# Performance work log

Hardware: AMD Instinct MI355X
Metric: run time of the kernel (lower is better)

## Reference

```python
import jax, jax.numpy as jnp
import numpy as np

RMS_EPS = 1e-8
Q_EPS = 1e-5

def rms_norm(x):
    # RMSNorm without learnable scale, as in BitNet reference BitLinear
    return x * jax.lax.rsqrt(jnp.mean(x * x, axis=-1, keepdims=True) + RMS_EPS)

def activation_quant(x):
    # per-token absmax int8 quant/dequant
    scale = 127.0 / jnp.clip(jnp.max(jnp.abs(x), axis=-1, keepdims=True), Q_EPS)
    return jnp.clip(jnp.round(x * scale), -128, 127) / scale

def weight_quant(w):
    # ternary absmean quant/dequant
    scale = 1.0 / jnp.clip(jnp.mean(jnp.abs(w)), Q_EPS)
    return jnp.clip(jnp.round(w * scale), -1, 1) / scale

def bitlinear(x, w):
    # forward path of BitLinear: RMSNorm -> quantized matmul (STE is identity in fwd)
    xn = rms_norm(x)
    xq = xn + jax.lax.stop_gradient(activation_quant(xn) - xn)
    wq = w + jax.lax.stop_gradient(weight_quant(w) - w)
    return jnp.einsum('bsh,oh->bso', xq, wq)

def setup_inputs() -> dict:
    key = jax.random.key(0)
    k1, k2, k3 = jax.random.split(key, 3)
    H, I = 2048, 8192  # hidden_size, intermediate_size = 4*H
    x = jax.random.normal(k1, (4, 2048, H), jnp.float32)
    w_gate = jax.random.normal(k2, (2 * I, H), jnp.float32) * 0.02
    w_down = jax.random.normal(k3, (H, I), jnp.float32) * 0.02
    return {"x": x, "w_gate": w_gate, "w_down": w_down}

def reference(x, w_gate, w_down):
    y = bitlinear(x, w_gate)          # [B,S,2I]
    gate, v = jnp.split(y, 2, axis=-1)
    return bitlinear(jax.nn.silu(gate) * v, w_down)  # [B,S,H]
```

## Files before the change

kernel.cpp:

```cpp
#include <hip/hip_runtime.h>


using char8  = __attribute__((ext_vector_type(8))) signed char;
using int4v  = __attribute__((ext_vector_type(4))) int;
using half8  = __attribute__((ext_vector_type(8))) _Float16;

__device__ __forceinline__ void glds16(const void* g, void* l) {
  __builtin_amdgcn_global_load_lds((const __attribute__((address_space(1))) void*)g,
                                   (__attribute__((address_space(3))) void*)l, 16, 0, 0);
}

#define SB0() __builtin_amdgcn_sched_barrier(0)

__global__ __launch_bounds__(256) void reduce_abs_kernel(
    const float4* __restrict__ w, float* __restrict__ partials, int n4) {
  int t = threadIdx.x;
  int gid = blockIdx.x * 256 + t;
  int stride = gridDim.x * 256;
  float s = 0.f;
  for (int i = gid; i < n4; i += stride) {
    float4 u = w[i];
    s += fabsf(u.x) + fabsf(u.y) + fabsf(u.z) + fabsf(u.w);
  }
  __shared__ float sm[256];
  sm[t] = s; __syncthreads();
  for (int off = 128; off > 0; off >>= 1) {
    if (t < off) sm[t] += sm[t + off];
    __syncthreads();
  }
  if (t == 0) partials[blockIdx.x] = sm[0];
}

__global__ __launch_bounds__(256) void finalize_kernel(
    const float* __restrict__ pf, float* __restrict__ scales) {
  __shared__ float sm[256];
  int t = threadIdx.x;
  float s = pf[t] + pf[t + 256] + pf[t + 512] + pf[t + 768];
  sm[t] = s; __syncthreads();
  for (int off = 128; off > 0; off >>= 1) {
    if (t < off) sm[t] += sm[t + off];
    __syncthreads();
  }
  if (t == 0) {
    float c = fmaxf(sm[0] / 33554432.0f, 1e-5f);
    scales[0] = c; scales[2] = 1.0f / c;
  }
  __syncthreads();
  s = pf[1024 + t] + pf[1280 + t] + pf[1536 + t] + pf[1792 + t];
  sm[t] = s; __syncthreads();
  for (int off = 128; off > 0; off >>= 1) {
    if (t < off) sm[t] += sm[t + off];
    __syncthreads();
  }
  if (t == 0) {
    float c = fmaxf(sm[0] / 16777216.0f, 1e-5f);
    scales[1] = c; scales[3] = 1.0f / c;
  }
}

__global__ __launch_bounds__(256) void quant_weight_kernel(
    const float4* __restrict__ w, char8* __restrict__ wq,
    const float* __restrict__ invp, int n8) {
  float inv = *invp;
  int stride = gridDim.x * 256;
  for (int i = blockIdx.x * 256 + threadIdx.x; i < n8; i += stride) {
    float4 a = w[2 * i], b = w[2 * i + 1];
    float v[8] = {a.x, a.y, a.z, a.w, b.x, b.y, b.z, b.w};
    char8 o;
#pragma unroll
    for (int j = 0; j < 8; ++j) {
      float q = rintf(v[j] * inv);
      q = fminf(fmaxf(q, -1.f), 1.f);
      o[j] = (signed char)(int)q;
    }
    wq[i] = o;
  }
}

__global__ __launch_bounds__(256) void act_quant_f32_kernel(
    const float* __restrict__ in, signed char* __restrict__ out,
    float* __restrict__ fscale) {
  const int token = blockIdx.x, t = threadIdx.x;
  const float4* row = (const float4*)(in + (size_t)token * 2048);
  float4 a = row[2 * t], b = row[2 * t + 1];
  float v[8] = {a.x, a.y, a.z, a.w, b.x, b.y, b.z, b.w};
  float ss = 0.f, am = 0.f;
#pragma unroll
  for (int j = 0; j < 8; ++j) { ss += v[j] * v[j]; am = fmaxf(am, fabsf(v[j])); }
  __shared__ float s1[256], s2[256];
  s1[t] = ss; s2[t] = am; __syncthreads();
  for (int off = 128; off > 0; off >>= 1) {
    if (t < off) { s1[t] += s1[t + off]; s2[t] = fmaxf(s2[t], s2[t + off]); }
    __syncthreads();
  }
  float r = 1.0f / sqrtf(s1[0] * (1.0f / 2048.0f) + 1e-8f);
  float f = fmaxf(s2[0] * r, 1e-5f);
  float s = 127.0f / f;
  if (t == 0) fscale[token] = f * (1.0f / 127.0f);
  char8 o;
#pragma unroll
  for (int j = 0; j < 8; ++j) {
    float q = rintf((v[j] * r) * s);
    q = fminf(fmaxf(q, -128.f), 127.f);
    o[j] = (signed char)(int)q;
  }
  ((char8*)(out + (size_t)token * 2048))[t] = o;
}

__global__ __launch_bounds__(256) void act_quant_h_kernel(
    const _Float16* __restrict__ in, signed char* __restrict__ out,
    float* __restrict__ fscale) {
  const int token = blockIdx.x, t = threadIdx.x;
  const half8* row = (const half8*)(in + (size_t)token * 8192);
  float v[32];
  float ss = 0.f, am = 0.f;
#pragma unroll
  for (int c = 0; c < 4; ++c) {
    half8 u = row[c * 256 + t];
#pragma unroll
    for (int j = 0; j < 8; ++j) {
      float f = (float)u[j]; v[c * 8 + j] = f;
      ss += f * f; am = fmaxf(am, fabsf(f));
    }
  }
  __shared__ float s1[256], s2[256];
  s1[t] = ss; s2[t] = am; __syncthreads();
  for (int off = 128; off > 0; off >>= 1) {
    if (t < off) { s1[t] += s1[t + off]; s2[t] = fmaxf(s2[t], s2[t + off]); }
    __syncthreads();
  }
  float r = 1.0f / sqrtf(s1[0] * (1.0f / 8192.0f) + 1e-8f);
  float f = fmaxf(s2[0] * r, 1e-5f);
  float s = 127.0f / f;
  if (t == 0) fscale[token] = f * (1.0f / 127.0f);
#pragma unroll
  for (int c = 0; c < 4; ++c) {
    char8 o;
#pragma unroll
    for (int j = 0; j < 8; ++j) {
      float q = rintf((v[c * 8 + j] * r) * s);
      q = fminf(fmaxf(q, -128.f), 127.f);
      o[j] = (signed char)(int)q;
    }
    ((char8*)(out + (size_t)token * 8192))[c * 256 + t] = o;
  }
}

__global__ __launch_bounds__(512, 2) void gemm1_kernel(
    const signed char* __restrict__ A,
    const signed char* __restrict__ B,
    const float* __restrict__ f1, const float* __restrict__ cgp,
    _Float16* __restrict__ Z) {
  constexpr int K = 2048, I = 8192, NT = K / 64;
  constexpr int ASZ = 16384, BUF = 32768;
  __shared__ __align__(16) signed char Ls[3 * BUF];
  const int t0 = blockIdx.y * 256, n0 = blockIdx.x * 128;
  const int tid = threadIdx.x, w = tid >> 6, l = tid & 63;
  const int wr = w >> 2, wc = w & 3;
  const int lrow = l & 15, lchunk = (l >> 4) * 16;

  int4v ag[8][2], av[8][2];
#pragma unroll
  for (int i = 0; i < 8; ++i)
#pragma unroll
    for (int j = 0; j < 2; ++j) { ag[i][j] = {0,0,0,0}; av[i][j] = {0,0,0,0}; }

  const signed char* src[4];
  int dst[4];
  src[0] = A + (size_t)(t0 + w * 16 + lrow) * K + lchunk;       dst[0] = w * 1024;
  src[1] = A + (size_t)(t0 + (w + 8) * 16 + lrow) * K + lchunk; dst[1] = (w + 8) * 1024;
  src[2] = B + (size_t)(n0 + w * 16 + lrow) * K + lchunk;       dst[2] = ASZ + w * 1024;
  src[3] = B + (size_t)(I + n0 + w * 16 + lrow) * K + lchunk;   dst[3] = ASZ + (8 + w) * 1024;

#pragma unroll
  for (int p = 0; p < 2; ++p)
#pragma unroll
    for (int r = 0; r < 4; ++r) glds16(src[r] + p * 64, &Ls[p * BUF + dst[r]]);
  asm volatile("s_waitcnt vmcnt(4)" ::: "memory");
  __builtin_amdgcn_s_barrier();
  SB0();

  const int abase = (8 * wr) * 1024 + l * 16;
  const int gbase = ASZ + (2 * wc) * 1024 + l * 16;
  const int vbase = ASZ + (8 + 2 * wc) * 1024 + l * 16;

  int curo = 0;
  for (int it = 0; it < NT; ++it) {
    int stgo = curo + 2 * BUF; if (stgo >= 3 * BUF) stgo -= 3 * BUF;
    const bool stg = (it + 2 < NT);
    const int ko = (it + 2) * 64;
    int4v bg0, bg1, bv0, bv1;

#pragma unroll
    for (int q = 0; q < 4; ++q) {
      int4v a0 = *(const int4v*)&Ls[curo + abase + (2 * q) * 1024];
      int4v a1 = *(const int4v*)&Ls[curo + abase + (2 * q + 1) * 1024];
      if (q == 0) {
        bg0 = *(const int4v*)&Ls[curo + gbase];
        bg1 = *(const int4v*)&Ls[curo + gbase + 1024];
        bv0 = *(const int4v*)&Ls[curo + vbase];
        bv1 = *(const int4v*)&Ls[curo + vbase + 1024];
      }
      if (stg) glds16(src[q] + ko, &Ls[stgo + dst[q]]);
      SB0();
      __builtin_amdgcn_s_barrier();
      asm volatile("s_waitcnt lgkmcnt(0)" ::: "memory");
      SB0();
      __builtin_amdgcn_s_setprio(1);
      ag[2*q  ][0] = __builtin_amdgcn_mfma_i32_16x16x64_i8(a0, bg0, ag[2*q  ][0], 0, 0, 0);
      ag[2*q  ][1] = __builtin_amdgcn_mfma_i32_16x16x64_i8(a0, bg1, ag[2*q  ][1], 0, 0, 0);
      av[2*q  ][0] = __builtin_amdgcn_mfma_i32_16x16x64_i8(a0, bv0, av[2*q  ][0], 0, 0, 0);
      av[2*q  ][1] = __builtin_amdgcn_mfma_i32_16x16x64_i8(a0, bv1, av[2*q  ][1], 0, 0, 0);
      ag[2*q+1][0] = __builtin_amdgcn_mfma_i32_16x16x64_i8(a1, bg0, ag[2*q+1][0], 0, 0, 0);
      ag[2*q+1][1] = __builtin_amdgcn_mfma_i32_16x16x64_i8(a1, bg1, ag[2*q+1][1], 0, 0, 0);
      av[2*q+1][0] = __builtin_amdgcn_mfma_i32_16x16x64_i8(a1, bv0, av[2*q+1][0], 0, 0, 0);
      av[2*q+1][1] = __builtin_amdgcn_mfma_i32_16x16x64_i8(a1, bv1, av[2*q+1][1], 0, 0, 0);
      __builtin_amdgcn_s_setprio(0);
      SB0();
      if (q < 3) {
        __builtin_amdgcn_s_barrier();
        SB0();
      }
    }
    if (it < NT - 2) asm volatile("s_waitcnt vmcnt(4)" ::: "memory");
    else             asm volatile("s_waitcnt vmcnt(0)" ::: "memory");
    __builtin_amdgcn_s_barrier();
    SB0();
    curo += BUF; if (curo == 3 * BUF) curo = 0;
  }

  float cg = *cgp;
#pragma unroll
  for (int i = 0; i < 8; ++i)
#pragma unroll
    for (int rr = 0; rr < 4; ++rr) {
      int m = 128 * wr + i * 16 + (l >> 4) * 4 + rr;
      float fs = f1[t0 + m] * cg;
#pragma unroll
      for (int j = 0; j < 2; ++j) {
        int n = 32 * wc + j * 16 + (l & 15);
        float g = (float)ag[i][j][rr] * fs, vv = (float)av[i][j][rr] * fs;
        float z = g / (1.0f + __expf(-g)) * vv;
        Z[(size_t)(t0 + m) * I + n0 + n] = (_Float16)z;
      }
    }
}

__global__ __launch_bounds__(512, 2) void gemm2_kernel(
    const signed char* __restrict__ A,
    const signed char* __restrict__ B,
    const float* __restrict__ f2, const float* __restrict__ cdp,
    float* __restrict__ out) {
  constexpr int K = 8192, N = 2048, NT = K / 64;
  constexpr int ASZ = 16384, BUF = 32768;
  __shared__ __align__(16) signed char Ls[3 * BUF];
  const int t0 = blockIdx.y * 256, n0 = blockIdx.x * 256;
  const int tid = threadIdx.x, w = tid >> 6, l = tid & 63;
  const int wr = w >> 2, wc = w & 3;
  const int lrow = l & 15, lchunk = (l >> 4) * 16;

  int4v acc[8][4];
#pragma unroll
  for (int i = 0; i < 8; ++i)
#pragma unroll
    for (int j = 0; j < 4; ++j) acc[i][j] = {0,0,0,0};

  const signed char* src[4];
  int dst[4];
  src[0] = A + (size_t)(t0 + w * 16 + lrow) * K + lchunk;       dst[0] = w * 1024;
  src[1] = A + (size_t)(t0 + (w + 8) * 16 + lrow) * K + lchunk; dst[1] = (w + 8) * 1024;
  src[2] = B + (size_t)(n0 + w * 16 + lrow) * K + lchunk;       dst[2] = ASZ + w * 1024;
  src[3] = B + (size_t)(n0 + (w + 8) * 16 + lrow) * K + lchunk; dst[3] = ASZ + (w + 8) * 1024;

#pragma unroll
  for (int p = 0; p < 2; ++p)
#pragma unroll
    for (int r = 0; r < 4; ++r) glds16(src[r] + p * 64, &Ls[p * BUF + dst[r]]);
  asm volatile("s_waitcnt vmcnt(4)" ::: "memory");
  __builtin_amdgcn_s_barrier();
  SB0();

  const int abase = (8 * wr) * 1024 + l * 16;
  const int bbase = ASZ + (4 * wc) * 1024 + l * 16;

  int curo = 0;
  for (int it = 0; it < NT; ++it) {
    int stgo = curo + 2 * BUF; if (stgo >= 3 * BUF) stgo -= 3 * BUF;
    const bool stg = (it + 2 < NT);
    const int ko = (it + 2) * 64;
    int4v bf0, bf1, bf2, bf3;

#pragma unroll
    for (int q = 0; q < 4; ++q) {
      int4v a0 = *(const int4v*)&Ls[curo + abase + (2 * q) * 1024];
      int4v a1 = *(const int4v*)&Ls[curo + abase + (2 * q + 1) * 1024];
      if (q == 0) {
        bf0 = *(const int4v*)&Ls[curo + bbase];
        bf1 = *(const int4v*)&Ls[curo + bbase + 1024];
        bf2 = *(const int4v*)&Ls[curo + bbase + 2048];
        bf3 = *(const int4v*)&Ls[curo + bbase + 3072];
      }
      if (stg) glds16(src[q] + ko, &Ls[stgo + dst[q]]);
      SB0();
      __builtin_amdgcn_s_barrier();
      asm volatile("s_waitcnt lgkmcnt(0)" ::: "memory");
      SB0();
      __builtin_amdgcn_s_setprio(1);
      acc[2*q  ][0] = __builtin_amdgcn_mfma_i32_16x16x64_i8(a0, bf0, acc[2*q  ][0], 0, 0, 0);
      acc[2*q  ][1] = __builtin_amdgcn_mfma_i32_16x16x64_i8(a0, bf1, acc[2*q  ][1], 0, 0, 0);
      acc[2*q  ][2] = __builtin_amdgcn_mfma_i32_16x16x64_i8(a0, bf2, acc[2*q  ][2], 0, 0, 0);
      acc[2*q  ][3] = __builtin_amdgcn_mfma_i32_16x16x64_i8(a0, bf3, acc[2*q  ][3], 0, 0, 0);
      acc[2*q+1][0] = __builtin_amdgcn_mfma_i32_16x16x64_i8(a1, bf0, acc[2*q+1][0], 0, 0, 0);
      acc[2*q+1][1] = __builtin_amdgcn_mfma_i32_16x16x64_i8(a1, bf1, acc[2*q+1][1], 0, 0, 0);
      acc[2*q+1][2] = __builtin_amdgcn_mfma_i32_16x16x64_i8(a1, bf2, acc[2*q+1][2], 0, 0, 0);
      acc[2*q+1][3] = __builtin_amdgcn_mfma_i32_16x16x64_i8(a1, bf3, acc[2*q+1][3], 0, 0, 0);
      __builtin_amdgcn_s_setprio(0);
      SB0();
      if (q < 3) {
        __builtin_amdgcn_s_barrier();
        SB0();
      }
    }
    if (it < NT - 2) asm volatile("s_waitcnt vmcnt(4)" ::: "memory");
    else             asm volatile("s_waitcnt vmcnt(0)" ::: "memory");
    __builtin_amdgcn_s_barrier();
    SB0();
    curo += BUF; if (curo == 3 * BUF) curo = 0;
  }

  float cd = *cdp;
#pragma unroll
  for (int i = 0; i < 8; ++i)
#pragma unroll
    for (int rr = 0; rr < 4; ++rr) {
      int m = 128 * wr + i * 16 + (l >> 4) * 4 + rr;
      float fs = f2[t0 + m] * cd;
#pragma unroll
      for (int j = 0; j < 4; ++j) {
        int n = 64 * wc + j * 16 + (l & 15);
        out[(size_t)(t0 + m) * N + n0 + n] = (float)acc[i][j][rr] * fs;
      }
    }
}

extern "C" void kernel_launch(void* const* d_in, const int* in_sizes, int n_in,
                              void* d_out, int out_size, void* d_ws, size_t ws_size,
                              hipStream_t stream) {
  const float* x  = (const float*)d_in[0];
  const float* wg = (const float*)d_in[1];
  const float* wd = (const float*)d_in[2];
  float* out = (float*)d_out;

  char* ws = (char*)d_ws;
  signed char* wgq = (signed char*)(ws);
  signed char* wdq = (signed char*)(ws + 33554432);
  signed char* xq  = (signed char*)(ws + 50331648);
  signed char* zq  = (signed char*)(ws + 67108864);
  _Float16*    z   = (_Float16*)  (ws + 134217728);
  float* f1     = (float*)(ws + 268435456);
  float* f2     = (float*)(ws + 268468224);
  float* pf     = (float*)(ws + 268500992);
  float* scales = (float*)(ws + 268509184);

  reduce_abs_kernel<<<1024, 256, 0, stream>>>((const float4*)wg, pf, 8388608);
  reduce_abs_kernel<<<1024, 256, 0, stream>>>((const float4*)wd, pf + 1024, 4194304);
  finalize_kernel<<<1, 256, 0, stream>>>(pf, scales);

  quant_weight_kernel<<<2048, 256, 0, stream>>>((const float4*)wg, (char8*)wgq, scales + 2, 4194304);
  quant_weight_kernel<<<1024, 256, 0, stream>>>((const float4*)wd, (char8*)wdq, scales + 3, 2097152);
  act_quant_f32_kernel<<<8192, 256, 0, stream>>>(x, xq, f1);

  gemm1_kernel<<<dim3(64, 32), 512, 0, stream>>>(xq, wgq, f1, scales, z);

  act_quant_h_kernel<<<8192, 256, 0, stream>>>(z, zq, f2);

  gemm2_kernel<<<dim3(8, 32), 512, 0, stream>>>(zq, wdq, f2, scales + 1, out);
}
```

Baseline: 804.2 us.

## Register-prefetch next K-tile LDS fragments and cut per-iteration barriers

Both int8 GEMM main loops now load every A/B LDS fragment for the next K-step into registers while the current step's MFMAs run. Each iteration splits its 32 MFMAs into two halves with the global-to-LDS staging loads issued between them. The four barriers per K-step drop to one, so LDS read latency is hidden behind matrix work. The cost is roughly twice the VGPRs for operand fragments, which could cause spills under the 512-thread, 2-blocks-per-SM launch bound. The barrier now sits between the writes and the reads of the next buffer, so its correctness depends on the triple-buffer ordering holding.

```diff
diff --git a/kernel.cpp b/kernel.cpp
--- a/kernel.cpp
+++ b/kernel.cpp
@@ -145,6 +145,8 @@
     ((char8*)(out + (size_t)token * 8192))[c * 256 + t] = o;
   }
 }
+
+#define RD1(off) (*(const int4v*)&Ls[(off)])
 
 __global__ __launch_bounds__(512, 2) void gemm1_kernel(
     const signed char* __restrict__ A,
@@ -184,49 +186,80 @@
   const int gbase = ASZ + (2 * wc) * 1024 + l * 16;
   const int vbase = ASZ + (8 + 2 * wc) * 1024 + l * 16;
 
+  int4v a0 = RD1(abase), a1 = RD1(abase + 1024), a2 = RD1(abase + 2048),
+        a3 = RD1(abase + 3072), a4 = RD1(abase + 4096), a5 = RD1(abase + 5120),
+        a6 = RD1(abase + 6144), a7 = RD1(abase + 7168);
+  int4v bg0 = RD1(gbase), bg1 = RD1(gbase + 1024);
+  int4v bv0 = RD1(vbase), bv1 = RD1(vbase + 1024);
+
   int curo = 0;
   for (int it = 0; it < NT; ++it) {
-    int stgo = curo + 2 * BUF; if (stgo >= 3 * BUF) stgo -= 3 * BUF;
-    const bool stg = (it + 2 < NT);
+    int nxto = curo + BUF; if (nxto == 3 * BUF) nxto = 0;
+    int stgo = nxto + BUF; if (stgo == 3 * BUF) stgo = 0;
+    const bool stg = (it <= NT - 3);
     const int ko = (it + 2) * 64;
-    int4v bg0, bg1, bv0, bv1;
-
-#pragma unroll
-    for (int q = 0; q < 4; ++q) {
-      int4v a0 = *(const int4v*)&Ls[curo + abase + (2 * q) * 1024];
-      int4v a1 = *(const int4v*)&Ls[curo + abase + (2 * q + 1) * 1024];
-      if (q == 0) {
-        bg0 = *(const int4v*)&Ls[curo + gbase];
-        bg1 = *(const int4v*)&Ls[curo + gbase + 1024];
-        bv0 = *(const int4v*)&Ls[curo + vbase];
-        bv1 = *(const int4v*)&Ls[curo + vbase + 1024];
-      }
-      if (stg) glds16(src[q] + ko, &Ls[stgo + dst[q]]);
+
+    if (stg) { glds16(src[0] + ko, &Ls[stgo + dst[0]]);
+               glds16(src[1] + ko, &Ls[stgo + dst[1]]); }
+    __builtin_amdgcn_s_setprio(1);
+    ag[0][0] = __builtin_amdgcn_mfma_i32_16x16x64_i8(a0, bg0, ag[0][0], 0, 0, 0);
+    ag[0][1] = __builtin_amdgcn_mfma_i32_16x16x64_i8(a0, bg1, ag[0][1], 0, 0, 0);
+    av[0][0] = __builtin_amdgcn_mfma_i32_16x16x64_i8(a0, bv0, av[0][0], 0, 0, 0);
+    av[0][1] = __builtin_amdgcn_mfma_i32_16x16x64_i8(a0, bv1, av[0][1], 0, 0, 0);
+    ag[1][0] = __builtin_amdgcn_mfma_i32_16x16x64_i8(a1, bg0, ag[1][0], 0, 0, 0);
+    ag[1][1] = __builtin_amdgcn_mfma_i32_16x16x64_i8(a1, bg1, ag[1][1], 0, 0, 0);
+    av[1][0] = __builtin_amdgcn_mfma_i32_16x16x64_i8(a1, bv0, av[1][0], 0, 0, 0);
+    av[1][1] = __builtin_amdgcn_mfma_i32_16x16x64_i8(a1, bv1, av[1][1], 0, 0, 0);
+    ag[2][0] = __builtin_amdgcn_mfma_i32_16x16x64_i8(a2, bg0, ag[2][0], 0, 0, 0);
+    ag[2][1] = __builtin_amdgcn_mfma_i32_16x16x64_i8(a2, bg1, ag[2][1], 0, 0, 0);
+    av[2][0] = __builtin_amdgcn_mfma_i32_16x16x64_i8(a2, bv0, av[2][0], 0, 0, 0);
+    av[2][1] = __builtin_amdgcn_mfma_i32_16x16x64_i8(a2, bv1, av[2][1], 0, 0, 0);
+    ag[3][0] = __builtin_amdgcn_mfma_i32_16x16x64_i8(a3, bg0, ag[3][0], 0, 0, 0);
+    ag[3][1] = __builtin_amdgcn_mfma_i32_16x16x64_i8(a3, bg1, ag[3][1], 0, 0, 0);
+    av[3][0] = __builtin_amdgcn_mfma_i32_16x16x64_i8(a3, bv0, av[3][0], 0, 0, 0);
+    av[3][1] = __builtin_amdgcn_mfma_i32_16x16x64_i8(a3, bv1, av[3][1], 0, 0, 0);
+    __builtin_amdgcn_s_setprio(0);
+
+    if (stg) { glds16(src[2] + ko, &Ls[stgo + dst[2]]);
+               glds16(src[3] + ko, &Ls[stgo + dst[3]]); }
+    if (it <= NT - 3)      asm volatile("s_waitcnt vmcnt(4)" ::: "memory");
+    else if (it == NT - 2) asm volatile("s_waitcnt vmcnt(0)" ::: "memory");
+    int4v na0, na1, na2, na3, na4, na5, na6, na7, nbg0, nbg1, nbv0, nbv1;
+    if (it + 1 < NT) {
+      __builtin_amdgcn_s_barrier();
       SB0();
-      __builtin_amdgcn_s_barrier();
-      asm volatile("s_waitcnt lgkmcnt(0)" ::: "memory");
-      SB0();
-      __builtin_amdgcn_s_setprio(1);
-      ag[2*q  ][0] = __builtin_amdgcn_mfma_i32_16x16x64_i8(a0, bg0, ag[2*q  ][0], 0, 0, 0);
-      ag[2*q  ][1] = __builtin_amdgcn_mfma_i32_16x16x64_i8(a0, bg1, ag[2*q  ][1], 0, 0, 0);
-      av[2*q  ][0] = __builtin_amdgcn_mfma_i32_16x16x64_i8(a0, bv0, av[2*q  ][0], 0, 0, 0);
-      av[2*q  ][1] = __builtin_amdgcn_mfma_i32_16x16x64_i8(a0, bv1, av[2*q  ][1], 0, 0, 0);
-      ag[2*q+1][0] = __builtin_amdgcn_mfma_i32_16x16x64_i8(a1, bg0, ag[2*q+1][0], 0, 0, 0);
-      ag[2*q+1][1] = __builtin_amdgcn_mfma_i32_16x16x64_i8(a1, bg1, ag[2*q+1][1], 0, 0, 0);
-      av[2*q+1][0] = __builtin_amdgcn_mfma_i32_16x16x64_i8(a1, bv0, av[2*q+1][0], 0, 0, 0);
-      av[2*q+1][1] = __builtin_amdgcn_mfma_i32_16x16x64_i8(a1, bv1, av[2*q+1][1], 0, 0, 0);
-      __builtin_amdgcn_s_setprio(0);
-      SB0();
-      if (q < 3) {
-        __builtin_amdgcn_s_barrier();
-        SB0();
-      }
-    }
-    if (it < NT - 2) asm volatile("s_waitcnt vmcnt(4)" ::: "memory");
-    else             asm volatile("s_waitcnt vmcnt(0)" ::: "memory");
-    __builtin_amdgcn_s_barrier();
-    SB0();
-    curo += BUF; if (curo == 3 * BUF) curo = 0;
+      na0 = RD1(nxto + abase);        na1 = RD1(nxto + abase + 1024);
+      na2 = RD1(nxto + abase + 2048); na3 = RD1(nxto + abase + 3072);
+      na4 = RD1(nxto + abase + 4096); na5 = RD1(nxto + abase + 5120);
+      na6 = RD1(nxto + abase + 6144); na7 = RD1(nxto + abase + 7168);
+      nbg0 = RD1(nxto + gbase); nbg1 = RD1(nxto + gbase + 1024);
+      nbv0 = RD1(nxto + vbase); nbv1 = RD1(nxto + vbase + 1024);
+    }
+    __builtin_amdgcn_s_setprio(1);
+    ag[4][0] = __builtin_amdgcn_mfma_i32_16x16x64_i8(a4, bg0, ag[4][0], 0, 0, 0);
+    ag[4][1] = __builtin_amdgcn_mfma_i32_16x16x64_i8(a4, bg1, ag[4][1], 0, 0, 0);
+    av[4][0] = __builtin_amdgcn_mfma_i32_16x16x64_i8(a4, bv0, av[4][0], 0, 0, 0);
+    av[4][1] = __builtin_amdgcn_mfma_i32_16x16x64_i8(a4, bv1, av[4][1], 0, 0, 0);
+    ag[5][0] = __builtin_amdgcn_mfma_i32_16x16x64_i8(a5, bg0, ag[5][0], 0, 0, 0);
+    ag[5][1] = __builtin_amdgcn_mfma_i32_16x16x64_i8(a5, bg1, ag[5][1], 0, 0, 0);
+    av[5][0] = __builtin_amdgcn_mfma_i32_16x16x64_i8(a5, bv0, av[5][0], 0, 0, 0);
+    av[5][1] = __builtin_amdgcn_mfma_i32_16x16x64_i8(a5, bv1, av[5][1], 0, 0, 0);
+    ag[6][0] = __builtin_amdgcn_mfma_i32_16x16x64_i8(a6, bg0, ag[6][0], 0, 0, 0);
+    ag[6][1] = __builtin_amdgcn_mfma_i32_16x16x64_i8(a6, bg1, ag[6][1], 0, 0, 0);
+    av[6][0] = __builtin_amdgcn_mfma_i32_16x16x64_i8(a6, bv0, av[6][0], 0, 0, 0);
+    av[6][1] = __builtin_amdgcn_mfma_i32_16x16x64_i8(a6, bv1, av[6][1], 0, 0, 0);
+    ag[7][0] = __builtin_amdgcn_mfma_i32_16x16x64_i8(a7, bg0, ag[7][0], 0, 0, 0);
+    ag[7][1] = __builtin_amdgcn_mfma_i32_16x16x64_i8(a7, bg1, ag[7][1], 0, 0, 0);
+    av[7][0] = __builtin_amdgcn_mfma_i32_16x16x64_i8(a7, bv0, av[7][0], 0, 0, 0);
+    av[7][1] = __builtin_amdgcn_mfma_i32_16x16x64_i8(a7, bv1, av[7][1], 0, 0, 0);
+    __builtin_amdgcn_s_setprio(0);
+
+    if (it + 1 < NT) {
+      a0 = na0; a1 = na1; a2 = na2; a3 = na3;
+      a4 = na4; a5 = na5; a6 = na6; a7 = na7;
+      bg0 = nbg0; bg1 = nbg1; bv0 = nbv0; bv1 = nbv1;
+    }
+    curo = nxto;
   }
 
   float cg = *cgp;
@@ -283,49 +316,80 @@
   const int abase = (8 * wr) * 1024 + l * 16;
   const int bbase = ASZ + (4 * wc) * 1024 + l * 16;
 
+  int4v a0 = RD1(abase), a1 = RD1(abase + 1024), a2 = RD1(abase + 2048),
+        a3 = RD1(abase + 3072), a4 = RD1(abase + 4096), a5 = RD1(abase + 5120),
+        a6 = RD1(abase + 6144), a7 = RD1(abase + 7168);
+  int4v b0 = RD1(bbase), b1 = RD1(bbase + 1024),
+        b2 = RD1(bbase + 2048), b3 = RD1(bbase + 3072);
+
   int curo = 0;
   for (int it = 0; it < NT; ++it) {
-    int stgo = curo + 2 * BUF; if (stgo >= 3 * BUF) stgo -= 3 * BUF;
-    const bool stg = (it + 2 < NT);
+    int nxto = curo + BUF; if (nxto == 3 * BUF) nxto = 0;
+    int stgo = nxto + BUF; if (stgo == 3 * BUF) stgo = 0;
+    const bool stg = (it <= NT - 3);
     const int ko = (it + 2) * 64;
-    int4v bf0, bf1, bf2, bf3;
-
-#pragma unroll
-    for (int q = 0; q < 4; ++q) {
-      int4v a0 = *(const int4v*)&Ls[curo + abase + (2 * q) * 1024];
-      int4v a1 = *(const int4v*)&Ls[curo + abase + (2 * q + 1) * 1024];
-      if (q == 0) {
-        bf0 = *(const int4v*)&Ls[curo + bbase];
-        bf1 = *(const int4v*)&Ls[curo + bbase + 1024];
-        bf2 = *(const int4v*)&Ls[curo + bbase + 2048];
-        bf3 = *(const int4v*)&Ls[curo + bbase + 3072];
-      }
-      if (stg) glds16(src[q] + ko, &Ls[stgo + dst[q]]);
+
+    if (stg) { glds16(src[0] + ko, &Ls[stgo + dst[0]]);
+               glds16(src[1] + ko, &Ls[stgo + dst[1]]); }
+    __builtin_amdgcn_s_setprio(1);
+    acc[0][0] = __builtin_amdgcn_mfma_i32_16x16x64_i8(a0, b0, acc[0][0], 0, 0, 0);
+    acc[0][1] = __builtin_amdgcn_mfma_i32_16x16x64_i8(a0, b1, acc[0][1], 0, 0, 0);
+    acc[0][2] = __builtin_amdgcn_mfma_i32_16x16x64_i8(a0, b2, acc[0][2], 0, 0, 0);
+    acc[0][3] = __builtin_amdgcn_mfma_i32_16x16x64_i8(a0, b3, acc[0][3], 0, 0, 0);
+    acc[1][0] = __builtin_amdgcn_mfma_i32_16x16x64_i8(a1, b0, acc[1][0], 0, 0, 0);
+    acc[1][1] = __builtin_amdgcn_mfma_i32_16x16x64_i8(a1, b1, acc[1][1], 0, 0, 0);
+    acc[1][2] = __builtin_amdgcn_mfma_i32_16x16x64_i8(a1, b2, acc[1][2], 0, 0, 0);
+    acc[1][3] = __builtin_amdgcn_mfma_i32_16x16x64_i8(a1, b3, acc[1][3], 0, 0, 0);
+    acc[2][0] = __builtin_amdgcn_mfma_i32_16x16x64_i8(a2, b0, acc[2][0], 0, 0, 0);
+    acc[2][1] = __builtin_amdgcn_mfma_i32_16x16x64_i8(a2, b1, acc[2][1], 0, 0, 0);
+    acc[2][2] = __builtin_amdgcn_mfma_i32_16x16x64_i8(a2, b2, acc[2][2], 0, 0, 0);
+    acc[2][3] = __builtin_amdgcn_mfma_i32_16x16x64_i8(a2, b3, acc[2][3], 0, 0, 0);
+    acc[3][0] = __builtin_amdgcn_mfma_i32_16x16x64_i8(a3, b0, acc[3][0], 0, 0, 0);
+    acc[3][1] = __builtin_amdgcn_mfma_i32_16x16x64_i8(a3, b1, acc[3][1], 0, 0, 0);
+    acc[3][2] = __builtin_amdgcn_mfma_i32_16x16x64_i8(a3, b2, acc[3][2], 0, 0, 0);
+    acc[3][3] = __builtin_amdgcn_mfma_i32_16x16x64_i8(a3, b3, acc[3][3], 0, 0, 0);
+    __builtin_amdgcn_s_setprio(0);
+
+    if (stg) { glds16(src[2] + ko, &Ls[stgo + dst[2]]);
+               glds16(src[3] + ko, &Ls[stgo + dst[3]]); }
+    if (it <= NT - 3)      asm volatile("s_waitcnt vmcnt(4)" ::: "memory");
+    else if (it == NT - 2) asm volatile("s_waitcnt vmcnt(0)" ::: "memory");
+    int4v na0, na1, na2, na3, na4, na5, na6, na7, nb0, nb1, nb2, nb3;
+    if (it + 1 < NT) {
+      __builtin_amdgcn_s_barrier();
       SB0();
-      __builtin_amdgcn_s_barrier();
-      asm volatile("s_waitcnt lgkmcnt(0)" ::: "memory");
-      SB0();
-      __builtin_amdgcn_s_setprio(1);
-      acc[2*q  ][0] = __builtin_amdgcn_mfma_i32_16x16x64_i8(a0, bf0, acc[2*q  ][0], 0, 0, 0);
-      acc[2*q  ][1] = __builtin_amdgcn_mfma_i32_16x16x64_i8(a0, bf1, acc[2*q  ][1], 0, 0, 0);
-      acc[2*q  ][2] = __builtin_amdgcn_mfma_i32_16x16x64_i8(a0, bf2, acc[2*q  ][2], 0, 0, 0);
-      acc[2*q  ][3] = __builtin_amdgcn_mfma_i32_16x16x64_i8(a0, bf3, acc[2*q  ][3], 0, 0, 0);
-      acc[2*q+1][0] = __builtin_amdgcn_mfma_i32_16x16x64_i8(a1, bf0, acc[2*q+1][0], 0, 0, 0);
-      acc[2*q+1][1] = __builtin_amdgcn_mfma_i32_16x16x64_i8(a1, bf1, acc[2*q+1][1], 0, 0, 0);
-      acc[2*q+1][2] = __builtin_amdgcn_mfma_i32_16x16x64_i8(a1, bf2, acc[2*q+1][2], 0, 0, 0);
-      acc[2*q+1][3] = __builtin_amdgcn_mfma_i32_16x16x64_i8(a1, bf3, acc[2*q+1][3], 0, 0, 0);
-      __builtin_amdgcn_s_setprio(0);
-      SB0();
-      if (q < 3) {
-        __builtin_amdgcn_s_barrier();
-        SB0();
-      }
-    }
-    if (it < NT - 2) asm volatile("s_waitcnt vmcnt(4)" ::: "memory");
-    else             asm volatile("s_waitcnt vmcnt(0)" ::: "memory");
-    __builtin_amdgcn_s_barrier();
-    SB0();
-    curo += BUF; if (curo == 3 * BUF) curo = 0;
+      na0 = RD1(nxto + abase);        na1 = RD1(nxto + abase + 1024);
+      na2 = RD1(nxto + abase + 2048); na3 = RD1(nxto + abase + 3072);
+      na4 = RD1(nxto + abase + 4096); na5 = RD1(nxto + abase + 5120);
+      na6 = RD1(nxto + abase + 6144); na7 = RD1(nxto + abase + 7168);
+      nb0 = RD1(nxto + bbase);        nb1 = RD1(nxto + bbase + 1024);
+      nb2 = RD1(nxto + bbase + 2048); nb3 = RD1(nxto + bbase + 3072);
+    }
+    __builtin_amdgcn_s_setprio(1);
+    acc[4][0] = __builtin_amdgcn_mfma_i32_16x16x64_i8(a4, b0, acc[4][0], 0, 0, 0);
+    acc[4][1] = __builtin_amdgcn_mfma_i32_16x16x64_i8(a4, b1, acc[4][1], 0, 0, 0);
+    acc[4][2] = __builtin_amdgcn_mfma_i32_16x16x64_i8(a4, b2, acc[4][2], 0, 0, 0);
+    acc[4][3] = __builtin_amdgcn_mfma_i32_16x16x64_i8(a4, b3, acc[4][3], 0, 0, 0);
+    acc[5][0] = __builtin_amdgcn_mfma_i32_16x16x64_i8(a5, b0, acc[5][0], 0, 0, 0);
+    acc[5][1] = __builtin_amdgcn_mfma_i32_16x16x64_i8(a5, b1, acc[5][1], 0, 0, 0);
+    acc[5][2] = __builtin_amdgcn_mfma_i32_16x16x64_i8(a5, b2, acc[5][2], 0, 0, 0);
+    acc[5][3] = __builtin_amdgcn_mfma_i32_16x16x64_i8(a5, b3, acc[5][3], 0, 0, 0);
+    acc[6][0] = __builtin_amdgcn_mfma_i32_16x16x64_i8(a6, b0, acc[6][0], 0, 0, 0);
+    acc[6][1] = __builtin_amdgcn_mfma_i32_16x16x64_i8(a6, b1, acc[6][1], 0, 0, 0);
+    acc[6][2] = __builtin_amdgcn_mfma_i32_16x16x64_i8(a6, b2, acc[6][2], 0, 0, 0);
+    acc[6][3] = __builtin_amdgcn_mfma_i32_16x16x64_i8(a6, b3, acc[6][3], 0, 0, 0);
+    acc[7][0] = __builtin_amdgcn_mfma_i32_16x16x64_i8(a7, b0, acc[7][0], 0, 0, 0);
+    acc[7][1] = __builtin_amdgcn_mfma_i32_16x16x64_i8(a7, b1, acc[7][1], 0, 0, 0);
+    acc[7][2] = __builtin_amdgcn_mfma_i32_16x16x64_i8(a7, b2, acc[7][2], 0, 0, 0);
+    acc[7][3] = __builtin_amdgcn_mfma_i32_16x16x64_i8(a7, b3, acc[7][3], 0, 0, 0);
+    __builtin_amdgcn_s_setprio(0);
+
+    if (it + 1 < NT) {
+      a0 = na0; a1 = na1; a2 = na2; a3 = na3;
+      a4 = na4; a5 = na5; a6 = na6; a7 = na7;
+      b0 = nb0; b1 = nb1; b2 = nb2; b3 = nb3;
+    }
+    curo = nxto;
   }
 
   float cd = *cdp;
```

Result: no change. 810.0 us (+0.7%).
